# Kernel tuning notes

Measured on AMD Instinct MI355X. Metric: run time of the kernel, lower is better.

Reference implementation:

```python
import jax, jax.numpy as jnp
import numpy as np

PAD = 1  # symmetric spatial padding (pad_H == pad_W enforced by the module)


def setup_inputs() -> dict:
    key = jax.random.key(0)
    k1, k2, k3 = jax.random.split(key, 3)
    N, C, F, H, W, HH, WW = 32, 128, 128, 32, 32, 3, 3
    x = jax.random.normal(k1, (N, C, H, W), dtype=jnp.float32)
    weight = jax.random.normal(k2, (F, C, HH, WW), dtype=jnp.float32) * 0.05
    bias = jax.random.normal(k3, (F,), dtype=jnp.float32) * 0.05
    return {"x": x, "weight": weight, "bias": bias}


def reference(x, weight, bias):
    # Conv2dfft forward, no compression (compress_rate=0, preserve_energy=100,
    # next_power2=False, stride=1, real_fft path).
    N, C, H, W = x.shape
    F, _, HH, WW = weight.shape
    pad = PAD
    out_H = H - HH + 1 + 2 * pad
    out_W = W - WW + 1 + 2 * pad
    HHH = max(out_H, HH)
    WWW = max(out_W, WW)
    init_H = H + 2 * pad + HHH - 1  # full linear-conv FFT size
    init_W = W + 2 * pad + WWW - 1
    # torch_pad(input, (pad_W, pad_W + fft_pad_W, pad_H, pad_H + fft_pad_H))
    xp = jnp.pad(x, ((0, 0), (0, 0), (pad, init_H - pad - H), (pad, init_W - pad - W)))
    # torch_pad(filter, (0, fft_pad_W, 0, fft_pad_H))
    wp = jnp.pad(weight, ((0, 0), (0, 0), (0, init_H - HH), (0, init_W - WW)))
    xf = jnp.fft.rfft2(xp)          # [N, C, init_H, init_W//2+1] complex
    wf = jnp.fft.rfft2(wp)          # [F, C, init_H, init_W//2+1] complex
    # Cross-correlation in frequency domain: xfft * conj(yfft), contracted
    # over input channels C per frequency bin. This is exactly the math of the
    # module's fast_multiply (3-real-mult complex product via matmul) applied
    # to the conjugated filter spectrum.
    of = jnp.einsum('nchw,fchw->nfhw', xf, jnp.conj(wf))
    out = jnp.fft.irfft2(of, s=(init_H, init_W))[..., :out_H, :out_W]
    return out + bias[None, :, None, None]
```

## Files before the change

kernel.cpp:

```cpp
#include <hip/hip_runtime.h>


typedef short bf16x8 __attribute__((ext_vector_type(8)));
typedef short bf16x4 __attribute__((ext_vector_type(4)));
typedef float f32x4  __attribute__((ext_vector_type(4)));

__device__ __forceinline__ short f2bf(float f) {
  unsigned u = __builtin_bit_cast(unsigned, f);
  u = (u + 0x7fffu + ((u >> 16) & 1u)) >> 16;
  return (short)u;
}

__global__ __launch_bounds__(256) void conv_wprep(const float* __restrict__ w,
                                                  short* __restrict__ bc2) {
  int tid = blockIdx.x * 256 + threadIdx.x;
  float v = w[tid];
  int f   = tid / 1152;
  int rem = tid - f * 1152;
  int c   = rem / 9;
  int tap = rem - c * 9;
  int dst = ((((c >> 5) * 9 + tap) * 8 + (f >> 4)) * 512)
          + (((c >> 3) & 3) * 16 + (f & 15)) * 8
          + (c & 7);
  bc2[dst] = f2bf(v);
}

__device__ __forceinline__ void load_af(bf16x8* dst, const short* __restrict__ bc2,
                                        int chunk, int p, int fsel, int lane) {
  const short* base = bc2 + (((chunk * 9 + p * 3) * 8 + fsel * 4) * 512) + lane * 8;
#pragma unroll
  for (int q = 0; q < 3; ++q)
#pragma unroll
    for (int mt = 0; mt < 4; ++mt)
      dst[q * 4 + mt] = *(const bf16x8*)(base + (q * 8 + mt) * 512);
}

__global__ __launch_bounds__(256, 1) void conv_main(
    const float* __restrict__ x, const short* __restrict__ bc2,
    const float* __restrict__ bias, float* __restrict__ out) {
  __shared__ __align__(16) short xs[2][6 * 34 * 40];

  const int t    = threadIdx.x;
  const int lane = t & 63;
  const int wv   = t >> 6;
  const int n_img = blockIdx.x >> 3;
  const int h0    = (blockIdx.x & 7) << 2;

  const int l15  = lane & 15;
  const int quad = lane >> 4;
  const int fsel   = wv & 1;
  const int f_off  = fsel * 64;
  const int s_rowb = (wv >> 1) * 2;

  const int w_ = t & 31;
  const int g  = t >> 5;
  const float* xb = x + n_img * 128 * 1024;

  bf16x8 afA[12], afB[12];
  load_af(afA, bc2, 0, 0, fsel, lane);

  if (t < 192) {
    int buf = t / 96, rem = t % 96;
    int r = rem / 16, rem2 = rem % 16;
    int colsel = rem2 / 8, q4 = rem2 % 8;
    *(int2*)&xs[buf][(r * 34 + colsel * 33) * 40 + q4 * 4] = make_int2(0, 0);
  }

  f32x4 acc[4][4] = {};
  float xv[24];

#pragma unroll
  for (int r = 0; r < 6; ++r) {
    int hr = h0 - 1 + r;
    bool ok = (unsigned)hr < 32u;
#pragma unroll
    for (int cc = 0; cc < 4; ++cc)
      xv[r * 4 + cc] = ok ? xb[((g * 4 + cc) * 32 + hr) * 32 + w_] : 0.f;
  }
#pragma unroll
  for (int r = 0; r < 6; ++r) {
    bf16x4 v = { f2bf(xv[r*4+0]), f2bf(xv[r*4+1]), f2bf(xv[r*4+2]), f2bf(xv[r*4+3]) };
    *(bf16x4*)&xs[0][(r * 34 + w_ + 1) * 40 + g * 4] = v;
  }
  __syncthreads();

#pragma unroll
  for (int chunk = 0; chunk < 4; ++chunk) {
    if (chunk < 3) {
#pragma unroll
      for (int r = 0; r < 6; ++r) {
        int hr = h0 - 1 + r;
        bool ok = (unsigned)hr < 32u;
#pragma unroll
        for (int cc = 0; cc < 4; ++cc)
          xv[r * 4 + cc] =
              ok ? xb[(((chunk + 1) * 32 + g * 4 + cc) * 32 + hr) * 32 + w_] : 0.f;
      }
    }
    const short* xbuf = xs[chunk & 1];
#pragma unroll
    for (int p = 0; p < 3; ++p) {
      const int grp = chunk * 3 + p;
      const bf16x8* cur = (grp & 1) ? afB : afA;
      bf16x8*       nxt = (grp & 1) ? afA : afB;
      if (grp < 11)
        load_af(nxt, bc2, (grp + 1) / 3, (grp + 1) % 3, fsel, lane);
#pragma unroll
      for (int q = 0; q < 3; ++q) {
        bf16x8 bfr[4];
#pragma unroll
        for (int nt = 0; nt < 4; ++nt) {
          int r   = s_rowb + (nt >> 1) + p;
          int col = (nt & 1) * 16 + l15 + q;
          bfr[nt] = *(const bf16x8*)&xbuf[(r * 34 + col) * 40 + quad * 8];
        }
#pragma unroll
        for (int mt = 0; mt < 4; ++mt)
#pragma unroll
          for (int nt = 0; nt < 4; ++nt)
            acc[mt][nt] = __builtin_amdgcn_mfma_f32_16x16x32_bf16(
                cur[q * 4 + mt], bfr[nt], acc[mt][nt], 0, 0, 0);
      }
    }
    if (chunk < 3) {
#pragma unroll
      for (int r = 0; r < 6; ++r) {
        bf16x4 v = { f2bf(xv[r*4+0]), f2bf(xv[r*4+1]), f2bf(xv[r*4+2]), f2bf(xv[r*4+3]) };
        *(bf16x4*)&xs[(chunk + 1) & 1][(r * 34 + w_ + 1) * 40 + g * 4] = v;
      }
      __syncthreads();
    }
  }

#pragma unroll
  for (int nt = 0; nt < 4; ++nt) {
    int h = h0 + s_rowb + (nt >> 1);
    int w_out = (nt & 1) * 16 + l15;
#pragma unroll
    for (int mt = 0; mt < 4; ++mt) {
#pragma unroll
      for (int reg = 0; reg < 4; ++reg) {
        int f = f_off + mt * 16 + quad * 4 + reg;
        out[((n_img * 128 + f) * 32 + h) * 32 + w_out] = acc[mt][nt][reg] + bias[f];
      }
    }
  }
}

extern "C" void kernel_launch(void* const* d_in, const int* in_sizes, int n_in,
                              void* d_out, int out_size, void* d_ws, size_t ws_size,
                              hipStream_t stream) {
  const float* x    = (const float*)d_in[0];
  const float* w    = (const float*)d_in[1];
  const float* bias = (const float*)d_in[2];
  float* out = (float*)d_out;
  short* bc2 = (short*)d_ws;

  conv_wprep<<<576, 256, 0, stream>>>(w, bc2);
  conv_main<<<256, 256, 0, stream>>>(x, bc2, bias, out);
}
```

Measured before the change: 87.48 us.

## Double threads per block to 512, giving each wave one output row

Raises the block size from 256 to 512 threads (8 waves). Each wave now computes one output row instead of two, which halves the accumulator and staging registers per thread, and the input staging loads are redistributed across the larger thread count. The aim is more waves per CU to hide latency, since only 256 blocks exist for the GPU's CUs. The cost is that each weight fragment loaded into registers now feeds half as many MFMAs, so weight-fragment global traffic per output doubles.

```diff
diff --git a/kernel.cpp b/kernel.cpp
--- a/kernel.cpp
+++ b/kernel.cpp
@@ -35,7 +35,7 @@
       dst[q * 4 + mt] = *(const bf16x8*)(base + (q * 8 + mt) * 512);
 }
 
-__global__ __launch_bounds__(256, 1) void conv_main(
+__global__ __launch_bounds__(512, 2) void conv_main(
     const float* __restrict__ x, const short* __restrict__ bc2,
     const float* __restrict__ bias, float* __restrict__ out) {
   __shared__ __align__(16) short xs[2][6 * 34 * 40];
@@ -48,9 +48,9 @@
 
   const int l15  = lane & 15;
   const int quad = lane >> 4;
-  const int fsel   = wv & 1;
-  const int f_off  = fsel * 64;
-  const int s_rowb = (wv >> 1) * 2;
+  const int fsel  = wv & 1;
+  const int f_off = fsel * 64;
+  const int s_row = wv >> 1;
 
   const int w_ = t & 31;
   const int g  = t >> 5;
@@ -66,21 +66,25 @@
     *(int2*)&xs[buf][(r * 34 + colsel * 33) * 40 + q4 * 4] = make_int2(0, 0);
   }
 
-  f32x4 acc[4][4] = {};
-  float xv[24];
+  f32x4 acc[4][2] = {};
+  float xv[12];
 
 #pragma unroll
-  for (int r = 0; r < 6; ++r) {
+  for (int i = 0; i < 3; ++i) {
+    int idx = i * 16 + g;
+    int r = idx >> 3, cq = idx & 7;
     int hr = h0 - 1 + r;
     bool ok = (unsigned)hr < 32u;
 #pragma unroll
     for (int cc = 0; cc < 4; ++cc)
-      xv[r * 4 + cc] = ok ? xb[((g * 4 + cc) * 32 + hr) * 32 + w_] : 0.f;
+      xv[i * 4 + cc] = ok ? xb[(cq * 4 + cc) * 1024 + hr * 32 + w_] : 0.f;
   }
 #pragma unroll
-  for (int r = 0; r < 6; ++r) {
-    bf16x4 v = { f2bf(xv[r*4+0]), f2bf(xv[r*4+1]), f2bf(xv[r*4+2]), f2bf(xv[r*4+3]) };
-    *(bf16x4*)&xs[0][(r * 34 + w_ + 1) * 40 + g * 4] = v;
+  for (int i = 0; i < 3; ++i) {
+    int idx = i * 16 + g;
+    int r = idx >> 3, cq = idx & 7;
+    bf16x4 v = { f2bf(xv[i*4+0]), f2bf(xv[i*4+1]), f2bf(xv[i*4+2]), f2bf(xv[i*4+3]) };
+    *(bf16x4*)&xs[0][(r * 34 + w_ + 1) * 40 + cq * 4] = v;
   }
   __syncthreads();
 
@@ -88,13 +92,15 @@
   for (int chunk = 0; chunk < 4; ++chunk) {
     if (chunk < 3) {
 #pragma unroll
-      for (int r = 0; r < 6; ++r) {
+      for (int i = 0; i < 3; ++i) {
+        int idx = i * 16 + g;
+        int r = idx >> 3, cq = idx & 7;
         int hr = h0 - 1 + r;
         bool ok = (unsigned)hr < 32u;
 #pragma unroll
         for (int cc = 0; cc < 4; ++cc)
-          xv[r * 4 + cc] =
-              ok ? xb[(((chunk + 1) * 32 + g * 4 + cc) * 32 + hr) * 32 + w_] : 0.f;
+          xv[i * 4 + cc] =
+              ok ? xb[((chunk + 1) * 32 + cq * 4 + cc) * 1024 + hr * 32 + w_] : 0.f;
       }
     }
     const short* xbuf = xs[chunk & 1];
@@ -107,35 +113,37 @@
         load_af(nxt, bc2, (grp + 1) / 3, (grp + 1) % 3, fsel, lane);
 #pragma unroll
       for (int q = 0; q < 3; ++q) {
-        bf16x8 bfr[4];
+        bf16x8 bfr[2];
 #pragma unroll
-        for (int nt = 0; nt < 4; ++nt) {
-          int r   = s_rowb + (nt >> 1) + p;
-          int col = (nt & 1) * 16 + l15 + q;
+        for (int nt = 0; nt < 2; ++nt) {
+          int r   = s_row + p;
+          int col = nt * 16 + l15 + q;
           bfr[nt] = *(const bf16x8*)&xbuf[(r * 34 + col) * 40 + quad * 8];
         }
 #pragma unroll
         for (int mt = 0; mt < 4; ++mt)
 #pragma unroll
-          for (int nt = 0; nt < 4; ++nt)
+          for (int nt = 0; nt < 2; ++nt)
             acc[mt][nt] = __builtin_amdgcn_mfma_f32_16x16x32_bf16(
                 cur[q * 4 + mt], bfr[nt], acc[mt][nt], 0, 0, 0);
       }
     }
     if (chunk < 3) {
 #pragma unroll
-      for (int r = 0; r < 6; ++r) {
-        bf16x4 v = { f2bf(xv[r*4+0]), f2bf(xv[r*4+1]), f2bf(xv[r*4+2]), f2bf(xv[r*4+3]) };
-        *(bf16x4*)&xs[(chunk + 1) & 1][(r * 34 + w_ + 1) * 40 + g * 4] = v;
+      for (int i = 0; i < 3; ++i) {
+        int idx = i * 16 + g;
+        int r = idx >> 3, cq = idx & 7;
+        bf16x4 v = { f2bf(xv[i*4+0]), f2bf(xv[i*4+1]), f2bf(xv[i*4+2]), f2bf(xv[i*4+3]) };
+        *(bf16x4*)&xs[(chunk + 1) & 1][(r * 34 + w_ + 1) * 40 + cq * 4] = v;
       }
       __syncthreads();
     }
   }
 
+  const int h = h0 + s_row;
 #pragma unroll
-  for (int nt = 0; nt < 4; ++nt) {
-    int h = h0 + s_rowb + (nt >> 1);
-    int w_out = (nt & 1) * 16 + l15;
+  for (int nt = 0; nt < 2; ++nt) {
+    int w_out = nt * 16 + l15;
 #pragma unroll
     for (int mt = 0; mt < 4; ++mt) {
 #pragma unroll
@@ -157,5 +165,5 @@
   short* bc2 = (short*)d_ws;
 
   conv_wprep<<<576, 256, 0, stream>>>(w, bc2);
-  conv_main<<<256, 256, 0, stream>>>(x, bc2, bias, out);
+  conv_main<<<256, 512, 0, stream>>>(x, bc2, bias, out);
 }
```

After: 88.60 us. No clear change (+1.3%).

## Stage all input channels in LDS upfront and triple-buffer weight fragments

Applied to the files above, without the earlier changes.

Instead of double-buffering one 32-channel input chunk per iteration, all four chunks are loaded into four LDS buffers before a single barrier. The three per-chunk barriers disappear and the main loop becomes a flat 12-group MFMA sequence. Weight fragments are now prefetched two groups ahead across three register buffers instead of one group ahead across two. The cost is a serialized upfront global load with no overlap with compute, roughly twice the LDS footprint (about 65 KB), and extra VGPR pressure from the third 12-entry fragment array.

```diff
diff --git a/kernel.cpp b/kernel.cpp
--- a/kernel.cpp
+++ b/kernel.cpp
@@ -26,8 +26,8 @@
 }
 
 __device__ __forceinline__ void load_af(bf16x8* dst, const short* __restrict__ bc2,
-                                        int chunk, int p, int fsel, int lane) {
-  const short* base = bc2 + (((chunk * 9 + p * 3) * 8 + fsel * 4) * 512) + lane * 8;
+                                        int grp, int fsel, int lane) {
+  const short* base = bc2 + ((grp * 3 * 8 + fsel * 4) * 512) + lane * 8;
 #pragma unroll
   for (int q = 0; q < 3; ++q)
 #pragma unroll
@@ -38,7 +38,7 @@
 __global__ __launch_bounds__(256, 1) void conv_main(
     const float* __restrict__ x, const short* __restrict__ bc2,
     const float* __restrict__ bias, float* __restrict__ out) {
-  __shared__ __align__(16) short xs[2][6 * 34 * 40];
+  __shared__ __align__(16) short xs[4][6 * 34 * 40];
 
   const int t    = threadIdx.x;
   const int lane = t & 63;
@@ -56,79 +56,68 @@
   const int g  = t >> 5;
   const float* xb = x + n_img * 128 * 1024;
 
-  bf16x8 afA[12], afB[12];
-  load_af(afA, bc2, 0, 0, fsel, lane);
+  bf16x8 af0[12], af1[12], af2[12];
+  load_af(af0, bc2, 0, fsel, lane);
+  load_af(af1, bc2, 1, fsel, lane);
 
-  if (t < 192) {
-    int buf = t / 96, rem = t % 96;
-    int r = rem / 16, rem2 = rem % 16;
-    int colsel = rem2 / 8, q4 = rem2 % 8;
-    *(int2*)&xs[buf][(r * 34 + colsel * 33) * 40 + q4 * 4] = make_int2(0, 0);
+#pragma unroll
+  for (int i = 0; i < 2; ++i) {
+    int idx = i * 256 + t;
+    if (idx < 384) {
+      int ch = idx / 96, rem = idx % 96;
+      int r = rem / 16, rem2 = rem % 16;
+      int col = (rem2 / 8) * 33, q4 = rem2 % 8;
+      *(int2*)&xs[ch][(r * 34 + col) * 40 + q4 * 4] = make_int2(0, 0);
+    }
   }
 
-  f32x4 acc[4][4] = {};
-  float xv[24];
-
 #pragma unroll
-  for (int r = 0; r < 6; ++r) {
-    int hr = h0 - 1 + r;
-    bool ok = (unsigned)hr < 32u;
+  for (int chunk = 0; chunk < 4; ++chunk) {
+    float xv[24];
 #pragma unroll
-    for (int cc = 0; cc < 4; ++cc)
-      xv[r * 4 + cc] = ok ? xb[((g * 4 + cc) * 32 + hr) * 32 + w_] : 0.f;
-  }
+    for (int r = 0; r < 6; ++r) {
+      int hr = h0 - 1 + r;
+      bool ok = (unsigned)hr < 32u;
 #pragma unroll
-  for (int r = 0; r < 6; ++r) {
-    bf16x4 v = { f2bf(xv[r*4+0]), f2bf(xv[r*4+1]), f2bf(xv[r*4+2]), f2bf(xv[r*4+3]) };
-    *(bf16x4*)&xs[0][(r * 34 + w_ + 1) * 40 + g * 4] = v;
+      for (int cc = 0; cc < 4; ++cc)
+        xv[r * 4 + cc] =
+            ok ? xb[((chunk * 32 + g * 4 + cc) * 32 + hr) * 32 + w_] : 0.f;
+    }
+#pragma unroll
+    for (int r = 0; r < 6; ++r) {
+      bf16x4 v = { f2bf(xv[r*4+0]), f2bf(xv[r*4+1]), f2bf(xv[r*4+2]), f2bf(xv[r*4+3]) };
+      *(bf16x4*)&xs[chunk][(r * 34 + w_ + 1) * 40 + g * 4] = v;
+    }
   }
   __syncthreads();
 
+  f32x4 acc[4][4] = {};
+
 #pragma unroll
-  for (int chunk = 0; chunk < 4; ++chunk) {
-    if (chunk < 3) {
+  for (int grp = 0; grp < 12; ++grp) {
+    const int chunk = grp / 3, p = grp % 3;
+    const bf16x8* cur = (grp % 3 == 0) ? af0 : (grp % 3 == 1) ? af1 : af2;
+    if (grp + 2 <= 11) {
+      bf16x8* nxt = ((grp + 2) % 3 == 0) ? af0
+                  : ((grp + 2) % 3 == 1) ? af1 : af2;
+      load_af(nxt, bc2, grp + 2, fsel, lane);
+    }
+    const short* xbuf = xs[chunk];
 #pragma unroll
-      for (int r = 0; r < 6; ++r) {
-        int hr = h0 - 1 + r;
-        bool ok = (unsigned)hr < 32u;
+    for (int q = 0; q < 3; ++q) {
+      bf16x8 bfr[4];
 #pragma unroll
-        for (int cc = 0; cc < 4; ++cc)
-          xv[r * 4 + cc] =
-              ok ? xb[(((chunk + 1) * 32 + g * 4 + cc) * 32 + hr) * 32 + w_] : 0.f;
+      for (int nt = 0; nt < 4; ++nt) {
+        int r   = s_rowb + (nt >> 1) + p;
+        int col = (nt & 1) * 16 + l15 + q;
+        bfr[nt] = *(const bf16x8*)&xbuf[(r * 34 + col) * 40 + quad * 8];
       }
-    }
-    const short* xbuf = xs[chunk & 1];
 #pragma unroll
-    for (int p = 0; p < 3; ++p) {
-      const int grp = chunk * 3 + p;
-      const bf16x8* cur = (grp & 1) ? afB : afA;
-      bf16x8*       nxt = (grp & 1) ? afA : afB;
-      if (grp < 11)
-        load_af(nxt, bc2, (grp + 1) / 3, (grp + 1) % 3, fsel, lane);
+      for (int mt = 0; mt < 4; ++mt)
 #pragma unroll
-      for (int q = 0; q < 3; ++q) {
-        bf16x8 bfr[4];
-#pragma unroll
-        for (int nt = 0; nt < 4; ++nt) {
-          int r   = s_rowb + (nt >> 1) + p;
-          int col = (nt & 1) * 16 + l15 + q;
-          bfr[nt] = *(const bf16x8*)&xbuf[(r * 34 + col) * 40 + quad * 8];
-        }
-#pragma unroll
-        for (int mt = 0; mt < 4; ++mt)
-#pragma unroll
-          for (int nt = 0; nt < 4; ++nt)
-            acc[mt][nt] = __builtin_amdgcn_mfma_f32_16x16x32_bf16(
-                cur[q * 4 + mt], bfr[nt], acc[mt][nt], 0, 0, 0);
-      }
-    }
-    if (chunk < 3) {
-#pragma unroll
-      for (int r = 0; r < 6; ++r) {
-        bf16x4 v = { f2bf(xv[r*4+0]), f2bf(xv[r*4+1]), f2bf(xv[r*4+2]), f2bf(xv[r*4+3]) };
-        *(bf16x4*)&xs[(chunk + 1) & 1][(r * 34 + w_ + 1) * 40 + g * 4] = v;
-      }
-      __syncthreads();
+        for (int nt = 0; nt < 4; ++nt)
+          acc[mt][nt] = __builtin_amdgcn_mfma_f32_16x16x32_bf16(
+              cur[q * 4 + mt], bfr[nt], acc[mt][nt], 0, 0, 0);
     }
   }
 
```

Result: slower. 91.75 us (+4.9%).
